# Kernel optimization log

Hardware: AMD Instinct MI355X
Metric: run time of the kernel (lower is better)

The kernel has to match this reference:

```python
import jax, jax.numpy as jnp
import numpy as np

T = 32.0                       # softmax temperature
THRESH = float(np.cos(np.pi * 40.0 / 180.0))  # cos(degree), degree=40
NEG_INF = -9.0e15


def setup_inputs() -> dict:
    key = jax.random.key(0)
    ks = jax.random.split(key, 11)
    B, C, D_IMG, D_ATT, H_ATT, H = 2048, 1000, 2048, 312, 128, 128
    def rn(k, shape, scale=1.0):
        return jax.random.normal(k, shape, dtype=jnp.float32) * scale
    return {
        "image_feats": rn(ks[0], (B, D_IMG)),
        "img_proto":   rn(ks[1], (C, D_IMG)),
        "attributes":  rn(ks[2], (C, D_ATT)),
        "unused":      0,
        # parameters
        "att_g":   rn(ks[3], (D_ATT, H_ATT), 0.05),
        "slim_w":  rn(ks[4], (D_IMG, D_ATT), 0.02),   # proto_slim weight (transposed torch layout)
        "slim_b":  rn(ks[5], (D_ATT,), 0.02),
        "img_w":   rn(ks[6], (D_IMG, H), 0.02),
        "proto_w": rn(ks[7], (2 * D_ATT, H), 0.02),   # att_dim + proto_red_dim = 624
        "proto_b": rn(ks[8], (1, H), 0.02),
        "fc_w":    rn(ks[9], (H, 1), 0.05),
        "fc_b":    rn(ks[10], (1,), 0.05),
    }


def reference(image_feats, img_proto, attributes, unused,
              att_g, slim_w, slim_b, img_w, proto_w, proto_b, fc_w, fc_b):
    # proto_slim: [C, D_img] -> [C, att_dim]
    proto_red = img_proto @ slim_w + slim_b

    # --- get_attention: cosine similarity among attribute projections ---
    g = attributes @ att_g                                   # [C, att_hC] (g == h in original)
    gn = g / jnp.clip(jnp.linalg.norm(g, axis=1, keepdims=True), 1e-12)
    sim = gn @ gn.T                                          # [C, C] cosine similarity
    raw = jnp.where(sim > THRESH, sim, NEG_INF)              # threshold mask
    attn = jax.nn.softmax(raw * T, axis=1)                   # [C, C]

    # --- propagate prototypes ---
    att_outs = attn @ attributes                             # [C, att_dim]
    img_proto_outs = attn @ proto_red                        # [C, att_dim]
    outs = jnp.concatenate([att_outs, img_proto_outs], axis=1)  # [C, 2*att_dim]

    # --- relation MLP (broadcast instead of materialized expand+matmul) ---
    img_h = image_feats @ img_w                              # [B, H]
    proto_h = outs @ proto_w                                 # [C, H]
    hidden = jax.nn.relu(img_h[:, None, :] + proto_h[None, :, :] + proto_b)  # [B, C, H]
    outputs = hidden @ fc_w + fc_b                           # [B, C, 1]
    return outputs[..., 0]                                   # [B, C]
```

## Files before the change

### kernel.cpp

```cpp
#include <hip/hip_runtime.h>

typedef unsigned short ushort_t;
typedef __bf16 bf16x8 __attribute__((ext_vector_type(8)));
typedef float f32x4 __attribute__((ext_vector_type(4)));
typedef float f32x2 __attribute__((ext_vector_type(2)));
typedef ushort_t us4 __attribute__((ext_vector_type(4)));

#define T_SOFT 32.0f
#define THRESH 0.76604444311897803f
#define SW 1048
#define SA 72

__device__ __forceinline__ ushort_t f2bf(float f) {
  union { float f; unsigned u; } x; x.f = f;
  unsigned r = (x.u + 0x7fffu + ((x.u >> 16) & 1u)) >> 16;
  return (ushort_t)r;
}
__device__ __forceinline__ float bf2f(ushort_t h) {
  union { unsigned u; float f; } x; x.u = ((unsigned)h) << 16; return x.f;
}

__device__ __forceinline__ us4 pack4(float4 x) {
  union { unsigned u[2]; us4 h; } r;
  union { float4 f; unsigned u[4]; } a;
  a.f = x;
  r.u[0] = __builtin_amdgcn_perm(a.u[1] + 0x8000u, a.u[0] + 0x8000u, 0x07060302u);
  r.u[1] = __builtin_amdgcn_perm(a.u[3] + 0x8000u, a.u[2] + 0x8000u, 0x07060302u);
  return r.h;
}

struct RL { float4 v[8]; };
__device__ __forceinline__ RL r_load(const float* __restrict__ src, int srs, int rowbase, int rowmax,
                                     int kbase, int climit, int tid) {
  RL o;
  int frow = tid >> 4, fk = (tid & 15) * 4;
  #pragma unroll
  for (int p = 0; p < 8; ++p) {
    int row = rowbase + frow + p * 16; if (row > rowmax) row = rowmax;
    int k = kbase + fk;
    float4 val = make_float4(0.f, 0.f, 0.f, 0.f);
    if (k < climit) val = *reinterpret_cast<const float4*>(src + (size_t)row * srs + k);
    o.v[p] = val;
  }
  return o;
}
__device__ __forceinline__ void r_store(const RL& o, ushort_t* __restrict__ dst, int tid) {
  int frow = tid >> 4, fk = (tid & 15) * 4;
  #pragma unroll
  for (int p = 0; p < 8; ++p)
    *reinterpret_cast<us4*>(dst + (size_t)(frow + p * 16) * SA + fk) = pack4(o.v[p]);
}

struct TL { float v[4][8]; };
__device__ __forceinline__ TL t_load(const float* __restrict__ src, int srs, int rbase, int rlimit,
                                     int nbase, int tid) {
  TL o;
  int kg = (tid >> 4) * 4, ns = (tid & 15) * 8;
  #pragma unroll
  for (int i = 0; i < 4; ++i) {
    int r = rbase + kg + i;
    float4 a = make_float4(0.f,0.f,0.f,0.f), c = make_float4(0.f,0.f,0.f,0.f);
    if (r < rlimit) {
      a = *reinterpret_cast<const float4*>(src + (size_t)r * srs + nbase + ns);
      c = *reinterpret_cast<const float4*>(src + (size_t)r * srs + nbase + ns + 4);
    }
    o.v[i][0]=a.x; o.v[i][1]=a.y; o.v[i][2]=a.z; o.v[i][3]=a.w;
    o.v[i][4]=c.x; o.v[i][5]=c.y; o.v[i][6]=c.z; o.v[i][7]=c.w;
  }
  return o;
}
__device__ __forceinline__ void t_store(const TL& o, ushort_t* __restrict__ dst, int tid) {
  int kg = (tid >> 4) * 4, ns = (tid & 15) * 8;
  #pragma unroll
  for (int j = 0; j < 8; ++j) {
    us4 w;
    w[0] = f2bf(o.v[0][j]); w[1] = f2bf(o.v[1][j]); w[2] = f2bf(o.v[2][j]); w[3] = f2bf(o.v[3][j]);
    *reinterpret_cast<us4*>(dst + (size_t)(ns + j) * SA + kg) = w;
  }
}

struct AL { bf16x8 v[4]; };
__device__ __forceinline__ AL a_load(const ushort_t* __restrict__ src, int srs, int kbase, int tid) {
  AL o;
  int hrow = tid >> 3, hk = (tid & 7) * 8;
  #pragma unroll
  for (int p = 0; p < 4; ++p)
    o.v[p] = *reinterpret_cast<const bf16x8*>(src + (size_t)(hrow + p * 32) * srs + kbase + hk);
  return o;
}
__device__ __forceinline__ void a_store(const AL& o, ushort_t* __restrict__ dst, int tid) {
  int hrow = tid >> 3, hk = (tid & 7) * 8;
  #pragma unroll
  for (int p = 0; p < 4; ++p)
    *reinterpret_cast<bf16x8*>(dst + (size_t)(hrow + p * 32) * SA + hk) = o.v[p];
}

__device__ __forceinline__ void mfma8(ushort_t* __restrict__ As, ushort_t* __restrict__ Bs,
                                      int tid, f32x4 acc[2][8]) {
  int lane = tid & 63, wv = tid >> 6;
  int l15 = lane & 15, quad = lane >> 4;
  #pragma unroll
  for (int kh = 0; kh < 2; ++kh) {
    bf16x8 af[2];
    #pragma unroll
    for (int pi = 0; pi < 2; ++pi)
      af[pi] = *reinterpret_cast<bf16x8*>(As + ((wv * 2 + pi) * 16 + l15) * SA + kh * 32 + quad * 8);
    #pragma unroll
    for (int ct = 0; ct < 8; ++ct) {
      bf16x8 bfr = *reinterpret_cast<bf16x8*>(Bs + (ct * 16 + l15) * SA + kh * 32 + quad * 8);
      acc[0][ct] = __builtin_amdgcn_mfma_f32_16x16x32_bf16(af[0], bfr, acc[0][ct], 0, 0, 0);
      acc[1][ct] = __builtin_amdgcn_mfma_f32_16x16x32_bf16(af[1], bfr, acc[1][ct], 0, 0, 0);
    }
  }
}

__global__ __launch_bounds__(256) void prep_k(
    const float* __restrict__ attributes, const float* __restrict__ att_g,
    ushort_t* __restrict__ gn_bf,
    const float* __restrict__ image_feats, const float* __restrict__ img_w,
    float* __restrict__ ihp,
    const float* __restrict__ proto_w, const float* __restrict__ slim_w,
    ushort_t* __restrict__ M2T,
    const float* __restrict__ slim_b, const float* __restrict__ proto_b,
    float* __restrict__ biasG, int* __restrict__ cnt) {
  __shared__ ushort_t As[128 * SA];
  __shared__ ushort_t Bs[128 * SA];
  int b = blockIdx.x, tid = threadIdx.x;
  if (b < 125) {
    __shared__ float a_lds[8][316];
    __shared__ float red2[8][2];
    int h = tid & 127;
    int c0 = b * 8;
    for (int idx = tid; idx < 8 * 312; idx += 256) {
      int r = idx / 312;
      int k = idx - r * 312;
      a_lds[r][k] = attributes[(c0 + r) * 312 + k];
    }
    __syncthreads();
    float acc[8] = {0.f,0.f,0.f,0.f,0.f,0.f,0.f,0.f};
    #pragma unroll 2
    for (int k = 0; k < 312; k += 4) {
      float w0 = att_g[(k + 0) * 128 + h];
      float w1 = att_g[(k + 1) * 128 + h];
      float w2 = att_g[(k + 2) * 128 + h];
      float w3 = att_g[(k + 3) * 128 + h];
      #pragma unroll
      for (int r = 0; r < 8; ++r) {
        float4 a4 = *reinterpret_cast<const float4*>(&a_lds[r][k]);
        acc[r] += a4.x * w0 + a4.y * w1 + a4.z * w2 + a4.w * w3;
      }
    }
    int lane = tid & 63, wvid = (tid >> 6) & 1;
    #pragma unroll
    for (int r = 0; r < 8; ++r) {
      float v = acc[r] * acc[r];
      #pragma unroll
      for (int off = 32; off > 0; off >>= 1) v += __shfl_xor(v, off, 64);
      if (lane == 0) red2[r][wvid] = v;
    }
    __syncthreads();
    #pragma unroll
    for (int r = 0; r < 8; ++r) {
      float nrm = fmaxf(sqrtf(red2[r][0] + red2[r][1]), 1e-12f);
      gn_bf[(c0 + r) * 128 + h] = f2bf(acc[r] / nrm);
    }
    return;
  }
  if (b == 125) {
    us4 z = {0, 0, 0, 0};
    *reinterpret_cast<us4*>(gn_bf + 1000 * 128 + tid * 4) = z;
    if (tid < 8) cnt[tid] = 0;
    if (tid < 128) {
      int h = tid;
      float acc = proto_b[h];
      for (int n = 0; n < 312; n += 4) {
        acc += slim_b[n + 0] * proto_w[(size_t)(312 + n) * 128 + h];
        acc += slim_b[n + 1] * proto_w[(size_t)(313 + n) * 128 + h];
        acc += slim_b[n + 2] * proto_w[(size_t)(314 + n) * 128 + h];
        acc += slim_b[n + 3] * proto_w[(size_t)(315 + n) * 128 + h];
      }
      biasG[h] = acc;
    }
    return;
  }
  int lane = tid & 63, wv = tid >> 6;
  int l15 = lane & 15, quad = lane >> 4;
  f32x4 acc[2][8];
  #pragma unroll
  for (int i = 0; i < 2; ++i)
    #pragma unroll
    for (int j = 0; j < 8; ++j) acc[i][j] = f32x4{0.f, 0.f, 0.f, 0.f};

  if (b < 254) {
    int q = b - 126;
    int tile = q >> 3, kc = q & 7;
    int r0 = tile * 128, k0 = kc * 256;
    RL ra = r_load(image_feats, 2048, r0, 2047, k0, 1 << 30, tid);
    TL tb = t_load(img_w, 128, k0, 2048, 0, tid);
    #pragma unroll
    for (int s = 0; s < 4; ++s) {
      if (s) __syncthreads();
      r_store(ra, As, tid);
      t_store(tb, Bs, tid);
      if (s + 1 < 4) {
        ra = r_load(image_feats, 2048, r0, 2047, k0 + (s + 1) * 64, 1 << 30, tid);
        tb = t_load(img_w, 128, k0 + (s + 1) * 64, 2048, 0, tid);
      }
      __syncthreads();
      mfma8(As, Bs, tid, acc);
    }
    float* Cp = ihp + (size_t)kc * 262144;
    #pragma unroll
    for (int pi = 0; pi < 2; ++pi)
      #pragma unroll
      for (int ct = 0; ct < 8; ++ct) {
        int col = ct * 16 + l15;
        #pragma unroll
        for (int r = 0; r < 4; ++r) {
          int row = r0 + (wv * 2 + pi) * 16 + quad * 4 + r;
          Cp[(size_t)row * 128 + col] = acc[pi][ct][r];
        }
      }
    return;
  }
  {
    int c0 = (b - 254) * 128;
    TL ta = t_load(proto_w, 128, 312, 624, 0, tid);
    RL rb = r_load(slim_w, 312, c0, 2047, 0, 312, tid);
    for (int s = 0; s < 5; ++s) {
      if (s) __syncthreads();
      t_store(ta, As, tid);
      r_store(rb, Bs, tid);
      if (s + 1 < 5) {
        ta = t_load(proto_w, 128, 312 + (s + 1) * 64, 624, 0, tid);
        rb = r_load(slim_w, 312, c0, 2047, (s + 1) * 64, 312, tid);
      }
      __syncthreads();
      mfma8(As, Bs, tid, acc);
    }
    #pragma unroll
    for (int pi = 0; pi < 2; ++pi)
      #pragma unroll
      for (int ct = 0; ct < 8; ++ct) {
        int col = c0 + ct * 16 + l15;
        #pragma unroll
        for (int r = 0; r < 4; ++r) {
          int row = (wv * 2 + pi) * 16 + quad * 4 + r;
          M2T[(size_t)row * 2048 + col] = f2bf(acc[pi][ct][r]);
        }
      }
  }
}

__global__ __launch_bounds__(256) void mid_k(
    const float* __restrict__ ihp, float* __restrict__ img_h,
    const ushort_t* __restrict__ M2T, const float* __restrict__ img_proto,
    const float* __restrict__ attributes, const float* __restrict__ proto_w,
    float* __restrict__ GT_part, const float* __restrict__ biasG,
    ushort_t* __restrict__ GT, int* __restrict__ cnt) {
  __shared__ ushort_t As[128 * SA];
  __shared__ ushort_t Bs[128 * SA];
  __shared__ int lastv;
  int b = blockIdx.x, tid = threadIdx.x;
  if (b < 128) {
    int t = b * 256 + tid;
    size_t base = (size_t)t * 8;
    #pragma unroll
    for (int g = 0; g < 2; ++g) {
      float4 s = *reinterpret_cast<const float4*>(ihp + base + g * 4);
      #pragma unroll
      for (int c = 1; c < 8; ++c) {
        float4 v = *reinterpret_cast<const float4*>(ihp + (size_t)c * 262144 + base + g * 4);
        s.x += v.x; s.y += v.y; s.z += v.z; s.w += v.w;
      }
      *reinterpret_cast<float4*>(img_h + base + g * 4) = s;
    }
    return;
  }
  int q = b - 128;
  int jt = q / 9, ch = q - jt * 9;
  int j0 = jt * 128;
  int lane = tid & 63, wv = tid >> 6;
  int l15 = lane & 15, quad = lane >> 4;
  f32x4 acc[2][8];
  #pragma unroll
  for (int i = 0; i < 2; ++i)
    #pragma unroll
    for (int j = 0; j < 8; ++j) acc[i][j] = f32x4{0.f, 0.f, 0.f, 0.f};
  if (ch == 0) {
    TL ta = t_load(proto_w, 128, 0, 312, 0, tid);
    RL rb = r_load(attributes, 312, j0, 999, 0, 312, tid);
    for (int s = 0; s < 5; ++s) {
      if (s) __syncthreads();
      t_store(ta, As, tid);
      r_store(rb, Bs, tid);
      if (s + 1 < 5) {
        ta = t_load(proto_w, 128, (s + 1) * 64, 312, 0, tid);
        rb = r_load(attributes, 312, j0, 999, (s + 1) * 64, 312, tid);
      }
      __syncthreads();
      mfma8(As, Bs, tid, acc);
    }
  } else {
    int k0 = (ch - 1) * 256;
    AL aa = a_load(M2T, 2048, k0, tid);
    RL rb = r_load(img_proto, 2048, j0, 999, k0, 1 << 30, tid);
    #pragma unroll
    for (int s = 0; s < 4; ++s) {
      if (s) __syncthreads();
      a_store(aa, As, tid);
      r_store(rb, Bs, tid);
      if (s + 1 < 4) {
        aa = a_load(M2T, 2048, k0 + (s + 1) * 64, tid);
        rb = r_load(img_proto, 2048, j0, 999, k0 + (s + 1) * 64, 1 << 30, tid);
      }
      __syncthreads();
      mfma8(As, Bs, tid, acc);
    }
  }
  float* dst = GT_part + (size_t)ch * 131072;
  #pragma unroll
  for (int pi = 0; pi < 2; ++pi)
    #pragma unroll
    for (int ct = 0; ct < 8; ++ct) {
      int col = j0 + ct * 16 + l15;
      #pragma unroll
      for (int r = 0; r < 4; ++r) {
        int row = (wv * 2 + pi) * 16 + quad * 4 + r;
        dst[(size_t)row * 1024 + col] = acc[pi][ct][r];
      }
    }
  __threadfence();
  if (tid == 0) lastv = atomicAdd(&cnt[jt], 1);
  __syncthreads();
  if (lastv == 8) {
    __threadfence();
    int row = tid >> 1;
    int cb = j0 + (tid & 1) * 64;
    float bg = biasG[row];
    #pragma unroll
    for (int e = 0; e < 16; ++e) {
      size_t off = (size_t)row * 1024 + cb + e * 4;
      float4 s = *reinterpret_cast<const float4*>(GT_part + off);
      #pragma unroll
      for (int c = 1; c < 9; ++c) {
        float4 v = *reinterpret_cast<const float4*>(GT_part + (size_t)c * 131072 + off);
        s.x += v.x; s.y += v.y; s.z += v.z; s.w += v.w;
      }
      s.x += bg; s.y += bg; s.z += bg; s.w += bg;
      *reinterpret_cast<us4*>(GT + off) = pack4(s);
    }
  }
}

__global__ __launch_bounds__(512) void attn6_k(
    const ushort_t* __restrict__ gn_bf, const ushort_t* __restrict__ GT,
    float* __restrict__ ph) {
  __shared__ ushort_t W[16 * SW];
  __shared__ float rsum[16];
  __shared__ int flags[63];
  int tid = threadIdx.x;
  int i0 = blockIdx.x * 16;
  int lane = tid & 63, wv = tid >> 6;
  int l15 = lane & 15, quad = lane >> 4;
  if (tid < 63) flags[tid] = 0;
  if (tid >= 64 && tid < 80) rsum[tid - 64] = 0.f;
  if (tid < 256) W[(tid >> 4) * SW + 1008 + (tid & 15)] = 0;
  __syncthreads();

  const ushort_t* abase = gn_bf + (size_t)(i0 + l15) * 128 + quad * 8;
  bf16x8 af0 = *reinterpret_cast<const bf16x8*>(abase);
  bf16x8 af1 = *reinterpret_cast<const bf16x8*>(abase + 32);
  bf16x8 af2 = *reinterpret_cast<const bf16x8*>(abase + 64);
  bf16x8 af3 = *reinterpret_cast<const bf16x8*>(abase + 96);
  float rs[4] = {0.f, 0.f, 0.f, 0.f};
  for (int jt = wv; jt < 63; jt += 8) {
    const ushort_t* bbase = gn_bf + (size_t)(jt * 16 + l15) * 128 + quad * 8;
    f32x4 d = {0.f, 0.f, 0.f, 0.f};
    d = __builtin_amdgcn_mfma_f32_16x16x32_bf16(af0, *reinterpret_cast<const bf16x8*>(bbase),      d, 0, 0, 0);
    d = __builtin_amdgcn_mfma_f32_16x16x32_bf16(af1, *reinterpret_cast<const bf16x8*>(bbase + 32), d, 0, 0, 0);
    d = __builtin_amdgcn_mfma_f32_16x16x32_bf16(af2, *reinterpret_cast<const bf16x8*>(bbase + 64), d, 0, 0, 0);
    d = __builtin_amdgcn_mfma_f32_16x16x32_bf16(af3, *reinterpret_cast<const bf16x8*>(bbase + 96), d, 0, 0, 0);
    int hot = 0;
    #pragma unroll
    for (int r = 0; r < 4; ++r) {
      float w = 0.f;
      if (d[r] > THRESH) { w = __expf(T_SOFT * (d[r] - 1.0f)); hot = 1; }
      ushort_t wb = f2bf(w);
      W[(quad * 4 + r) * SW + jt * 16 + l15] = wb;
      rs[r] += bf2f(wb);
    }
    if (hot) flags[jt] = 1;
  }
  #pragma unroll
  for (int r = 0; r < 4; ++r) {
    float v = rs[r];
    v += __shfl_xor(v, 1, 64); v += __shfl_xor(v, 2, 64);
    v += __shfl_xor(v, 4, 64); v += __shfl_xor(v, 8, 64);
    if (l15 == 0) atomicAdd(&rsum[quad * 4 + r], v);
  }
  __syncthreads();

  f32x4 acc2 = {0.f, 0.f, 0.f, 0.f};
  int h = wv * 16 + l15;
  for (int s = 0; s < 32; ++s) {
    int f = flags[2 * s] | ((2 * s + 1 < 63) ? flags[2 * s + 1] : 0);
    if (!f) continue;
    bf16x8 a = *reinterpret_cast<bf16x8*>(W + l15 * SW + s * 32 + quad * 8);
    bf16x8 bfr = *reinterpret_cast<const bf16x8*>(GT + (size_t)h * 1024 + s * 32 + quad * 8);
    acc2 = __builtin_amdgcn_mfma_f32_16x16x32_bf16(a, bfr, acc2, 0, 0, 0);
  }
  #pragma unroll
  for (int r = 0; r < 4; ++r) {
    int row = quad * 4 + r;
    int gi = i0 + row;
    float inv = 1.f / fmaxf(rsum[row], 1e-30f);
    if (gi < 1000) ph[(size_t)gi * 128 + h] = acc2[r] * inv;
  }
}

__global__ __launch_bounds__(256) void final_k(
    const float* __restrict__ img_h, const float* __restrict__ ph,
    const float* __restrict__ fc_w, const float* __restrict__ fc_b,
    float* __restrict__ out) {
  __shared__ float ih[64][132];
  __shared__ float ps[64][132];
  __shared__ float ws_[128];
  int tid = threadIdx.x;
  int b0 = blockIdx.x * 64;
  int c0 = blockIdx.y * 64;
  for (int idx = tid; idx < 2048; idx += 256) {
    int row = idx >> 5, c4 = (idx & 31) * 4;
    float4 v = *reinterpret_cast<const float4*>(img_h + (size_t)(b0 + row) * 128 + c4);
    *reinterpret_cast<float4*>(&ih[row][c4]) = v;
  }
  for (int idx = tid; idx < 2048; idx += 256) {
    int row = idx >> 5, c4 = (idx & 31) * 4;
    int c = c0 + row;
    float4 v = make_float4(0.f, 0.f, 0.f, 0.f);
    if (c < 1000) v = *reinterpret_cast<const float4*>(ph + (size_t)c * 128 + c4);
    *reinterpret_cast<float4*>(&ps[row][c4]) = v;
  }
  if (tid < 128) ws_[tid] = fc_w[tid];
  __syncthreads();
  int tx = tid & 15, ty = tid >> 4;
  f32x2 acc[4][4] = {};
  const f32x2 zero2 = {0.f, 0.f};
  for (int h = 0; h < 128; h += 4) {
    float4 w4 = *reinterpret_cast<float4*>(&ws_[h]);
    f32x2 wlo = {w4.x, w4.y}, whi = {w4.z, w4.w};
    float4 a4[4], p4[4];
    #pragma unroll
    for (int i = 0; i < 4; ++i) a4[i] = *reinterpret_cast<float4*>(&ih[ty * 4 + i][h]);
    #pragma unroll
    for (int j = 0; j < 4; ++j) p4[j] = *reinterpret_cast<float4*>(&ps[tx * 4 + j][h]);
    #pragma unroll
    for (int i = 0; i < 4; ++i) {
      f32x2 alo = {a4[i].x, a4[i].y}, ahi = {a4[i].z, a4[i].w};
      #pragma unroll
      for (int j = 0; j < 4; ++j) {
        f32x2 plo = {p4[j].x, p4[j].y}, phi = {p4[j].z, p4[j].w};
        f32x2 t0 = __builtin_elementwise_max(alo + plo, zero2);
        f32x2 t1 = __builtin_elementwise_max(ahi + phi, zero2);
        acc[i][j] = acc[i][j] + t0 * wlo;
        acc[i][j] = acc[i][j] + t1 * whi;
      }
    }
  }
  float fb = fc_b[0];
  #pragma unroll
  for (int i = 0; i < 4; ++i) {
    int b = b0 + ty * 4 + i;
    int c = c0 + tx * 4;
    if (c < 1000) {
      float4 v = make_float4(acc[i][0].x + acc[i][0].y + fb, acc[i][1].x + acc[i][1].y + fb,
                             acc[i][2].x + acc[i][2].y + fb, acc[i][3].x + acc[i][3].y + fb);
      *reinterpret_cast<float4*>(out + (size_t)b * 1000 + c) = v;
    }
  }
}

extern "C" void kernel_launch(void* const* d_in, const int* in_sizes, int n_in,
                              void* d_out, int out_size, void* d_ws, size_t ws_size,
                              hipStream_t stream) {
  const float* image_feats = (const float*)d_in[0];
  const float* img_proto   = (const float*)d_in[1];
  const float* attributes  = (const float*)d_in[2];
  const float* att_g   = (const float*)d_in[4];
  const float* slim_w  = (const float*)d_in[5];
  const float* slim_b  = (const float*)d_in[6];
  const float* img_w   = (const float*)d_in[7];
  const float* proto_w = (const float*)d_in[8];
  const float* proto_b = (const float*)d_in[9];
  const float* fc_w    = (const float*)d_in[10];
  const float* fc_b    = (const float*)d_in[11];
  float* out = (float*)d_out;

  char* ws = (char*)d_ws;
  size_t o = 0;
  auto alloc = [&](size_t bytes) { size_t r = o; o += (bytes + 255) & ~(size_t)255; return r; };
  ushort_t* gn_bf   = (ushort_t*)(ws + alloc(1008ull * 128 * 2));
  ushort_t* M2T     = (ushort_t*)(ws + alloc(128ull * 2048 * 2));
  ushort_t* GT      = (ushort_t*)(ws + alloc(128ull * 1024 * 2));
  float* biasG     = (float*)(ws + alloc(128ull * 4));
  float* ihp       = (float*)(ws + alloc(8ull * 2048 * 128 * 4));
  float* GT_part   = (float*)(ws + alloc(9ull * 128 * 1024 * 4));
  float* img_h     = (float*)(ws + alloc(2048ull * 128 * 4));
  float* ph        = (float*)(ws + alloc(1000ull * 128 * 4));
  int*   cnt       = (int*)(ws + alloc(256));

  prep_k<<<270, 256, 0, stream>>>(attributes, att_g, gn_bf,
                                  image_feats, img_w, ihp,
                                  proto_w, slim_w, M2T,
                                  slim_b, proto_b, biasG, cnt);

  mid_k<<<200, 256, 0, stream>>>(ihp, img_h, M2T, img_proto,
                                 attributes, proto_w, GT_part, biasG, GT, cnt);

  attn6_k<<<63, 512, 0, stream>>>(gn_bf, GT, ph);

  final_k<<<dim3(32, 16), 256, 0, stream>>>(img_h, ph, fc_w, fc_b, out);
}
```

Measured before the change: 192.1 us.

## Replace atomic last-block reduction with separate reduce kernel and move attr GEMM earlier

Moves the proto_w×attributes partial GEMM (chunk 0) into the first kernel, since it has no dependency on M2T. The atomic counter and last-block reduction in the middle kernel are replaced by a separate gtred_k kernel that sums the nine partials and adds the bias. This removes the threadfence/atomic serialization and the tail where one block reduces alone. The cost is an extra kernel launch and one more global round trip.

```diff
diff --git a/kernel.cpp b/kernel.cpp
--- a/kernel.cpp
+++ b/kernel.cpp
@@ -120,9 +120,9 @@
     const float* __restrict__ image_feats, const float* __restrict__ img_w,
     float* __restrict__ ihp,
     const float* __restrict__ proto_w, const float* __restrict__ slim_w,
-    ushort_t* __restrict__ M2T,
+    ushort_t* __restrict__ M2T, float* __restrict__ GT_part,
     const float* __restrict__ slim_b, const float* __restrict__ proto_b,
-    float* __restrict__ biasG, int* __restrict__ cnt) {
+    float* __restrict__ biasG) {
   __shared__ ushort_t As[128 * SA];
   __shared__ ushort_t Bs[128 * SA];
   int b = blockIdx.x, tid = threadIdx.x;
@@ -169,18 +169,18 @@
   if (b == 125) {
     us4 z = {0, 0, 0, 0};
     *reinterpret_cast<us4*>(gn_bf + 1000 * 128 + tid * 4) = z;
-    if (tid < 8) cnt[tid] = 0;
-    if (tid < 128) {
-      int h = tid;
-      float acc = proto_b[h];
-      for (int n = 0; n < 312; n += 4) {
-        acc += slim_b[n + 0] * proto_w[(size_t)(312 + n) * 128 + h];
-        acc += slim_b[n + 1] * proto_w[(size_t)(313 + n) * 128 + h];
-        acc += slim_b[n + 2] * proto_w[(size_t)(314 + n) * 128 + h];
-        acc += slim_b[n + 3] * proto_w[(size_t)(315 + n) * 128 + h];
-      }
-      biasG[h] = acc;
-    }
+    return;
+  }
+  if (b == 126) {
+    int h = tid & 127;
+    float acc = proto_b[h];
+    for (int n = 0; n < 312; n += 4) {
+      acc += slim_b[n + 0] * proto_w[(size_t)(312 + n) * 128 + h];
+      acc += slim_b[n + 1] * proto_w[(size_t)(313 + n) * 128 + h];
+      acc += slim_b[n + 2] * proto_w[(size_t)(314 + n) * 128 + h];
+      acc += slim_b[n + 3] * proto_w[(size_t)(315 + n) * 128 + h];
+    }
+    if (tid < 128) biasG[h] = acc;
     return;
   }
   int lane = tid & 63, wv = tid >> 6;
@@ -191,8 +191,8 @@
     #pragma unroll
     for (int j = 0; j < 8; ++j) acc[i][j] = f32x4{0.f, 0.f, 0.f, 0.f};
 
-  if (b < 254) {
-    int q = b - 126;
+  if (b < 255) {
+    int q = b - 127;
     int tile = q >> 3, kc = q & 7;
     int r0 = tile * 128, k0 = kc * 256;
     RL ra = r_load(image_feats, 2048, r0, 2047, k0, 1 << 30, tid);
@@ -223,8 +223,8 @@
       }
     return;
   }
-  {
-    int c0 = (b - 254) * 128;
+  if (b < 271) {
+    int c0 = (b - 255) * 128;
     TL ta = t_load(proto_w, 128, 312, 624, 0, tid);
     RL rb = r_load(slim_w, 312, c0, 2047, 0, 312, tid);
     for (int s = 0; s < 5; ++s) {
@@ -249,45 +249,10 @@
           M2T[(size_t)row * 2048 + col] = f2bf(acc[pi][ct][r]);
         }
       }
-  }
-}
-
-__global__ __launch_bounds__(256) void mid_k(
-    const float* __restrict__ ihp, float* __restrict__ img_h,
-    const ushort_t* __restrict__ M2T, const float* __restrict__ img_proto,
-    const float* __restrict__ attributes, const float* __restrict__ proto_w,
-    float* __restrict__ GT_part, const float* __restrict__ biasG,
-    ushort_t* __restrict__ GT, int* __restrict__ cnt) {
-  __shared__ ushort_t As[128 * SA];
-  __shared__ ushort_t Bs[128 * SA];
-  __shared__ int lastv;
-  int b = blockIdx.x, tid = threadIdx.x;
-  if (b < 128) {
-    int t = b * 256 + tid;
-    size_t base = (size_t)t * 8;
-    #pragma unroll
-    for (int g = 0; g < 2; ++g) {
-      float4 s = *reinterpret_cast<const float4*>(ihp + base + g * 4);
-      #pragma unroll
-      for (int c = 1; c < 8; ++c) {
-        float4 v = *reinterpret_cast<const float4*>(ihp + (size_t)c * 262144 + base + g * 4);
-        s.x += v.x; s.y += v.y; s.z += v.z; s.w += v.w;
-      }
-      *reinterpret_cast<float4*>(img_h + base + g * 4) = s;
-    }
     return;
   }
-  int q = b - 128;
-  int jt = q / 9, ch = q - jt * 9;
-  int j0 = jt * 128;
-  int lane = tid & 63, wv = tid >> 6;
-  int l15 = lane & 15, quad = lane >> 4;
-  f32x4 acc[2][8];
-  #pragma unroll
-  for (int i = 0; i < 2; ++i)
-    #pragma unroll
-    for (int j = 0; j < 8; ++j) acc[i][j] = f32x4{0.f, 0.f, 0.f, 0.f};
-  if (ch == 0) {
+  {
+    int j0 = (b - 271) * 128;
     TL ta = t_load(proto_w, 128, 0, 312, 0, tid);
     RL rb = r_load(attributes, 312, j0, 999, 0, 312, tid);
     for (int s = 0; s < 5; ++s) {
@@ -301,24 +266,67 @@
       __syncthreads();
       mfma8(As, Bs, tid, acc);
     }
-  } else {
-    int k0 = (ch - 1) * 256;
-    AL aa = a_load(M2T, 2048, k0, tid);
-    RL rb = r_load(img_proto, 2048, j0, 999, k0, 1 << 30, tid);
-    #pragma unroll
-    for (int s = 0; s < 4; ++s) {
-      if (s) __syncthreads();
-      a_store(aa, As, tid);
-      r_store(rb, Bs, tid);
-      if (s + 1 < 4) {
-        aa = a_load(M2T, 2048, k0 + (s + 1) * 64, tid);
-        rb = r_load(img_proto, 2048, j0, 999, k0 + (s + 1) * 64, 1 << 30, tid);
-      }
-      __syncthreads();
-      mfma8(As, Bs, tid, acc);
-    }
-  }
-  float* dst = GT_part + (size_t)ch * 131072;
+    #pragma unroll
+    for (int pi = 0; pi < 2; ++pi)
+      #pragma unroll
+      for (int ct = 0; ct < 8; ++ct) {
+        int col = j0 + ct * 16 + l15;
+        #pragma unroll
+        for (int r = 0; r < 4; ++r) {
+          int row = (wv * 2 + pi) * 16 + quad * 4 + r;
+          GT_part[(size_t)row * 1024 + col] = acc[pi][ct][r];
+        }
+      }
+  }
+}
+
+__global__ __launch_bounds__(256) void red_k(
+    const float* __restrict__ ihp, float* __restrict__ img_h,
+    const ushort_t* __restrict__ M2T, const float* __restrict__ img_proto,
+    float* __restrict__ GT_part) {
+  __shared__ ushort_t As[128 * SA];
+  __shared__ ushort_t Bs[128 * SA];
+  int b = blockIdx.x, tid = threadIdx.x;
+  if (b < 128) {
+    int t = b * 256 + tid;
+    size_t base = (size_t)t * 8;
+    #pragma unroll
+    for (int g = 0; g < 2; ++g) {
+      float4 s = *reinterpret_cast<const float4*>(ihp + base + g * 4);
+      #pragma unroll
+      for (int c = 1; c < 8; ++c) {
+        float4 v = *reinterpret_cast<const float4*>(ihp + (size_t)c * 262144 + base + g * 4);
+        s.x += v.x; s.y += v.y; s.z += v.z; s.w += v.w;
+      }
+      *reinterpret_cast<float4*>(img_h + base + g * 4) = s;
+    }
+    return;
+  }
+  int q = b - 128;
+  int jt = q >> 3, ch = q & 7;
+  int j0 = jt * 128, k0 = ch * 256;
+  f32x4 acc[2][8];
+  #pragma unroll
+  for (int i = 0; i < 2; ++i)
+    #pragma unroll
+    for (int j = 0; j < 8; ++j) acc[i][j] = f32x4{0.f, 0.f, 0.f, 0.f};
+  AL aa = a_load(M2T, 2048, k0, tid);
+  RL rb = r_load(img_proto, 2048, j0, 999, k0, 1 << 30, tid);
+  #pragma unroll
+  for (int s = 0; s < 4; ++s) {
+    if (s) __syncthreads();
+    a_store(aa, As, tid);
+    r_store(rb, Bs, tid);
+    if (s + 1 < 4) {
+      aa = a_load(M2T, 2048, k0 + (s + 1) * 64, tid);
+      rb = r_load(img_proto, 2048, j0, 999, k0 + (s + 1) * 64, 1 << 30, tid);
+    }
+    __syncthreads();
+    mfma8(As, Bs, tid, acc);
+  }
+  int lane = tid & 63, wv = tid >> 6;
+  int l15 = lane & 15, quad = lane >> 4;
+  float* dst = GT_part + (size_t)(ch + 1) * 131072;
   #pragma unroll
   for (int pi = 0; pi < 2; ++pi)
     #pragma unroll
@@ -330,26 +338,25 @@
         dst[(size_t)row * 1024 + col] = acc[pi][ct][r];
       }
     }
-  __threadfence();
-  if (tid == 0) lastv = atomicAdd(&cnt[jt], 1);
-  __syncthreads();
-  if (lastv == 8) {
-    __threadfence();
-    int row = tid >> 1;
-    int cb = j0 + (tid & 1) * 64;
-    float bg = biasG[row];
-    #pragma unroll
-    for (int e = 0; e < 16; ++e) {
-      size_t off = (size_t)row * 1024 + cb + e * 4;
-      float4 s = *reinterpret_cast<const float4*>(GT_part + off);
-      #pragma unroll
-      for (int c = 1; c < 9; ++c) {
-        float4 v = *reinterpret_cast<const float4*>(GT_part + (size_t)c * 131072 + off);
-        s.x += v.x; s.y += v.y; s.z += v.z; s.w += v.w;
-      }
-      s.x += bg; s.y += bg; s.z += bg; s.w += bg;
-      *reinterpret_cast<us4*>(GT + off) = pack4(s);
-    }
+}
+
+__global__ __launch_bounds__(256) void gtred_k(const float* __restrict__ GT_part,
+                                               const float* __restrict__ biasG,
+                                               ushort_t* __restrict__ GT) {
+  int t = blockIdx.x * 256 + threadIdx.x;
+  size_t base = (size_t)t * 16;
+  int row = (int)(base >> 10);
+  float bg = biasG[row];
+  #pragma unroll
+  for (int g = 0; g < 4; ++g) {
+    float4 s = *reinterpret_cast<const float4*>(GT_part + base + g * 4);
+    #pragma unroll
+    for (int c = 1; c < 9; ++c) {
+      float4 v = *reinterpret_cast<const float4*>(GT_part + (size_t)c * 131072 + base + g * 4);
+      s.x += v.x; s.y += v.y; s.z += v.z; s.w += v.w;
+    }
+    s.x += bg; s.y += bg; s.z += bg; s.w += bg;
+    *reinterpret_cast<us4*>(GT + base + g * 4) = pack4(s);
   }
 }
 
@@ -507,15 +514,15 @@
   float* GT_part   = (float*)(ws + alloc(9ull * 128 * 1024 * 4));
   float* img_h     = (float*)(ws + alloc(2048ull * 128 * 4));
   float* ph        = (float*)(ws + alloc(1000ull * 128 * 4));
-  int*   cnt       = (int*)(ws + alloc(256));
-
-  prep_k<<<270, 256, 0, stream>>>(attributes, att_g, gn_bf,
+
+  prep_k<<<279, 256, 0, stream>>>(attributes, att_g, gn_bf,
                                   image_feats, img_w, ihp,
-                                  proto_w, slim_w, M2T,
-                                  slim_b, proto_b, biasG, cnt);
-
-  mid_k<<<200, 256, 0, stream>>>(ihp, img_h, M2T, img_proto,
-                                 attributes, proto_w, GT_part, biasG, GT, cnt);
+                                  proto_w, slim_w, M2T, GT_part,
+                                  slim_b, proto_b, biasG);
+
+  red_k<<<192, 256, 0, stream>>>(ihp, img_h, M2T, img_proto, GT_part);
+
+  gtred_k<<<32, 256, 0, stream>>>(GT_part, biasG, GT);
 
   attn6_k<<<63, 512, 0, stream>>>(gn_bf, GT, ph);
 
```

After: 160.6 us. -16.4%, faster.
